# Kernel tuning notes

Measured on AMD Instinct MI355X. Metric: run time of the kernel, lower is better.

The kernel has to match this reference:

```python
import jax, jax.numpy as jnp
import numpy as np

H = 1024
W = 1024
FID = 100          # palette_fidelity
NF = 8             # number of IFS functions in the FunctionSet stub
N_POINTS = 1 << 20
K_STEPS = 20


def setup_inputs() -> dict:
    key = jax.random.key(0)
    ks = jax.random.split(key, 8)
    # xy ~ Normal(0, initial_sigma=2.0), c ~ Uniform(0,1)
    xy = 2.0 * jax.random.normal(ks[0], (N_POINTS, 2), dtype=jnp.float32)
    c = jax.random.uniform(ks[1], (N_POINTS, 1), dtype=jnp.float32)
    points = jnp.concatenate([xy, c], axis=1)                      # [N,3]
    # per-step random function selection (external FunctionSet randomness)
    choices = jax.random.randint(ks[2], (K_STEPS, N_POINTS), 0, NF, dtype=jnp.int32)
    # contractive-ish affine maps
    A = 0.5 * jax.random.normal(ks[3], (NF, 2, 2), dtype=jnp.float32)
    b = jax.random.normal(ks[4], (NF, 2), dtype=jnp.float32)
    func_colors = jax.random.uniform(ks[5], (NF,), dtype=jnp.float32)
    palette = jax.random.uniform(ks[6], (FID + 1, 4), dtype=jnp.float32)
    # view window [-3,3]x[-3,3] -> min_vec / range_vec exactly as in __init__
    x_min, x_max, y_min, y_max = -3.0, 3.0, -3.0, 3.0
    min_vec = jnp.array([x_min, y_min], dtype=jnp.float32)
    range_vec = jnp.array([W / (x_max - x_min), H / (y_max - y_min)], dtype=jnp.float32)
    raw_image0 = jnp.zeros((4, H, W), dtype=jnp.float32)
    return dict(points=points, choices=choices, A=A, b=b,
                func_colors=func_colors, palette=palette,
                min_vec=min_vec, range_vec=range_vec,
                raw_image0=raw_image0, skip_first_k=2)


def reference(points, choices, A, b, func_colors, palette,
              min_vec, range_vec, raw_image0, skip_first_k):
    def step(carry, inputs):
        pts, img = carry
        k, idx = inputs                                   # idx: [N] function ids
        xy, c = pts[:, :2], pts[:, 2]
        # FunctionSet: per-point affine map + color blend (flame IFS)
        new_xy = jnp.einsum('nij,nj->ni', A[idx], xy) + b[idx]
        new_c = 0.5 * (c + func_colors[idx])
        pts = jnp.concatenate([new_xy, new_c[:, None]], axis=1)
        # palette interpolation (matches floor/ceil lerp in the original)
        _c = new_c * FID
        cf = jnp.floor(_c)
        cc = jnp.ceil(_c)
        t = (_c - cf)[:, None]
        cfi = jnp.clip(cf, 0, FID).astype(jnp.int32)
        cci = jnp.clip(cc, 0, FID).astype(jnp.int32)
        color_vectors = t * palette[cci] + (1.0 - t) * palette[cfi]   # [N,4]
        # bin indices: ((xy - min) * range).long()  (truncation toward zero)
        bins = ((new_xy - min_vec) * range_vec).astype(jnp.int32)
        xb, yb = bins[:, 0], bins[:, 1]
        ok = (xb >= 0) & (xb < W) & (yb >= 0) & (yb < H) & (k >= skip_first_k)
        xb = jnp.where(ok, xb, 0)
        yb = jnp.where(ok, yb, 0)
        vals = jnp.where(ok[:, None], color_vectors, 0.0)             # [N,4]
        # original indexes raw_image[color][x_bins, y_bins]
        img = img.at[:, xb, yb].add(vals.T)
        return (pts, img), None

    k_steps = choices.shape[0]
    (_, img), _ = jax.lax.scan(step, (points, raw_image0),
                               (jnp.arange(k_steps), choices))
    return img
```

## Files before the change

### kernel.cpp

```cpp
#include <hip/hip_runtime.h>

constexpr int H = 1024, W = 1024, FID = 100, NF = 8;
constexpr int NPTS = 1 << 20, KSTEPS = 20;
constexpr int HW = H * W;

constexpr int NTX = 16, NTY = 32, NTILES = NTX * NTY;
constexpr int TPIX = 64 * 32;
constexpr int NBLK = 2048;
constexpr int PPB = NPTS / NBLK;
constexpr int PPT = PPB / 256;
constexpr int NBLK_C = 1024;
constexpr int SEG_N = NTILES * NBLK;
constexpr int CHUNK = 16384;
constexpr int TH    = 16384;
constexpr int MAXREC = NPTS * KSTEPS;
constexpr int K4_GRID = MAXREC / CHUNK;
constexpr int K4_BS  = 512;
constexpr int MAXVIS = K4_GRID + NTILES;
constexpr unsigned INV = 0xFFFFFFFFu;
constexpr float QSCALE = 16384.0f;
constexpr float QINV   = 1.0f / 16384.0f;
constexpr float FXS  = 131072.0f;
constexpr float FXSI = 1.0f / 131072.0f;

__device__ __forceinline__ void decode_rec(unsigned r, const float4* sPal,
                                           int& pix, float& v0, float& v1,
                                           float& v2, float& v3) {
    pix = (int)(r & 2047u);
    const float _c = (float)(r >> 11) * QINV;
    const float cf = floorf(_c);
    const float tt = _c - cf;
    const int cfi = (int)fminf(fmaxf(cf, 0.f), (float)FID);
    const int cci = (int)fminf(fmaxf(ceilf(_c), 0.f), (float)FID);
    const float4 pc = sPal[cci];
    const float4 pf = sPal[cfi];
    const float omt = 1.f - tt;
    v0 = tt * pc.x + omt * pf.x;
    v1 = tt * pc.y + omt * pf.y;
    v2 = tt * pc.z + omt * pf.z;
    v3 = tt * pc.w + omt * pf.w;
}

__device__ __forceinline__ unsigned long long pack2(float a, float b) {
    const unsigned ua = __float2uint_rn(a * FXS);
    const unsigned ub = __float2uint_rn(b * FXS);
    return (unsigned long long)ua | ((unsigned long long)ub << 32);
}

__global__ __launch_bounds__(256)
void count_kernel(const float* __restrict__ points,
                  const int* __restrict__ choices,
                  const float* __restrict__ A,
                  const float* __restrict__ b,
                  const float* __restrict__ minv,
                  const float* __restrict__ rangev,
                  const int* __restrict__ skipp,
                  unsigned* __restrict__ hist,
                  unsigned long long* __restrict__ packed)
{
    __shared__ float sA[NF * 4], sB[NF * 2];
    __shared__ unsigned shist[4][NTILES];
    const int t = threadIdx.x;
    if (t < NF * 4) sA[t] = A[t];
    if (t < NF * 2) sB[t] = b[t];
    for (int i = t; i < 4 * NTILES; i += 256) ((unsigned*)shist)[i] = 0u;
    __syncthreads();

    const int blk = blockIdx.x;
    const int base = blk * 1024;
    const int n0 = base + 4 * t;
    const float mx = minv[0], my = minv[1], rx = rangev[0], ry = rangev[1];
    const int skip = skipp[0];
    const int wv = t >> 6;

    const float4 f0 = *(const float4*)&points[3 * n0 + 0];
    const float4 f1 = *(const float4*)&points[3 * n0 + 4];
    const float4 f2 = *(const float4*)&points[3 * n0 + 8];
    float px_[4] = { f0.x, f0.w, f1.z, f2.y };
    float py_[4] = { f0.y, f1.x, f1.w, f2.z };

    unsigned long long pk_[4] = { 0ull, 0ull, 0ull, 0ull };
    unsigned ctile_[4] = { INV, INV, INV, INV };
    unsigned ccnt_[4]  = { 0u, 0u, 0u, 0u };

#pragma unroll
    for (int k = 0; k < KSTEPS; ++k) {
        const int4 cv = *(const int4*)&choices[k * NPTS + n0];
        const int idxs[4] = { cv.x & 7, cv.y & 7, cv.z & 7, cv.w & 7 };
#pragma unroll
        for (int j = 0; j < 4; ++j) {
            const int idx = idxs[j];
            pk_[j] |= (unsigned long long)idx << (3 * k);
            const float nx = sA[idx*4+0]*px_[j] + sA[idx*4+1]*py_[j] + sB[idx*2+0];
            const float ny = sA[idx*4+2]*px_[j] + sA[idx*4+3]*py_[j] + sB[idx*2+1];
            px_[j] = nx; py_[j] = ny;
            const int xb = (int)((nx - mx) * rx);
            const int yb = (int)((ny - my) * ry);
            if (k >= skip && (unsigned)xb < (unsigned)W && (unsigned)yb < (unsigned)H) {
                const unsigned tile = (unsigned)(((xb >> 6) << 5) | (yb >> 5));
                if (tile == ctile_[j]) { ++ccnt_[j]; }
                else {
                    if (ctile_[j] != INV) atomicAdd(&shist[wv][ctile_[j]], ccnt_[j]);
                    ctile_[j] = tile; ccnt_[j] = 1;
                }
            }
        }
    }
#pragma unroll
    for (int j = 0; j < 4; ++j) {
        if (ctile_[j] != INV) atomicAdd(&shist[wv][ctile_[j]], ccnt_[j]);
        packed[n0 + j] = pk_[j];
    }
    __syncthreads();
    for (int tt = t; tt < NTILES; tt += 256) {
        hist[tt * NBLK + 2 * blk]     = shist[0][tt] + shist[1][tt];
        hist[tt * NBLK + 2 * blk + 1] = shist[2][tt] + shist[3][tt];
    }
}

__global__ __launch_bounds__(1024)
void scan1_kernel(unsigned* __restrict__ hist, unsigned* __restrict__ sums)
{
    __shared__ unsigned buf[2][1024];
    const int t = threadIdx.x;
    const int base = blockIdx.x * NBLK;
    const unsigned v0 = hist[base + 2 * t];
    const unsigned v1 = hist[base + 2 * t + 1];
    int src = 0;
    buf[0][t] = v0 + v1; __syncthreads();
    for (int off = 1; off < 1024; off <<= 1) {
        unsigned val = buf[src][t];
        if (t >= off) val += buf[src][t - off];
        buf[1 - src][t] = val; src ^= 1; __syncthreads();
    }
    const unsigned incl = buf[src][t];
    const unsigned ex = incl - (v0 + v1);
    hist[base + 2 * t]     = ex;
    hist[base + 2 * t + 1] = ex + v0;
    if (t == 1023) sums[blockIdx.x] = incl;
}

__global__ __launch_bounds__(512)
void scan2v_kernel(unsigned* __restrict__ sums,
                   unsigned* __restrict__ dstart,
                   unsigned* __restrict__ vstart)
{
    __shared__ unsigned buf[2][512];
    const int t = threadIdx.x;
    const unsigned len = sums[t];

    int src = 0;
    buf[0][t] = len; __syncthreads();
    for (int off = 1; off < 512; off <<= 1) {
        unsigned val = buf[src][t];
        if (t >= off) val += buf[src][t - off];
        buf[1 - src][t] = val; src ^= 1; __syncthreads();
    }
    unsigned incl = buf[src][t];
    sums[t] = incl - len;
    if (t == 511) sums[512] = incl;

    const unsigned dlen = (len >= (unsigned)TH) ? len : 0u;
    __syncthreads();
    buf[0][t] = dlen; src = 0; __syncthreads();
    for (int off = 1; off < 512; off <<= 1) {
        unsigned val = buf[src][t];
        if (t >= off) val += buf[src][t - off];
        buf[1 - src][t] = val; src ^= 1; __syncthreads();
    }
    unsigned dincl = buf[src][t];
    const unsigned dexcl = dincl - dlen;
    dstart[t] = dexcl;
    if (t == 511) dstart[512] = dincl;

    unsigned c = 0;
    if (dlen) c = (dexcl + dlen - 1) / CHUNK - dexcl / CHUNK + 1;
    __syncthreads();
    buf[0][t] = c; src = 0; __syncthreads();
    for (int off = 1; off < 512; off <<= 1) {
        unsigned val = buf[src][t];
        if (t >= off) val += buf[src][t - off];
        buf[1 - src][t] = val; src ^= 1; __syncthreads();
    }
    unsigned vincl = buf[src][t];
    vstart[t] = vincl - c;
    if (t == 511) vstart[512] = vincl;
}

__global__ __launch_bounds__(256)
void scatter_kernel(const float* __restrict__ points,
                    const unsigned long long* __restrict__ packed,
                    const float* __restrict__ A,
                    const float* __restrict__ b,
                    const float* __restrict__ fc,
                    const float* __restrict__ minv,
                    const float* __restrict__ rangev,
                    const int* __restrict__ skipp,
                    const unsigned* __restrict__ scanb,
                    const unsigned* __restrict__ sums,
                    unsigned* __restrict__ records)
{
    __shared__ float sA[NF * 4], sB[NF * 2], sFC[NF];
    __shared__ unsigned sCur[NTILES];

    const int t = threadIdx.x;
    const int blk = blockIdx.x;
    if (t < NF * 4) sA[t] = A[t];
    if (t < NF * 2) sB[t] = b[t];
    if (t < NF)     sFC[t] = fc[t];
    for (int tt = t; tt < NTILES; tt += 256)
        sCur[tt] = scanb[tt * NBLK + blk] + sums[tt];
    __syncthreads();

    const int base = blk * PPB;
    const float mx = minv[0], my = minv[1], rx = rangev[0], ry = rangev[1];
    const int skip = skipp[0];

    for (int p = 0; p < PPT; ++p) {
        const int n = base + p * 256 + t;
        float x = points[3*n], y = points[3*n+1], c = points[3*n+2];
        const unsigned long long pk = packed[n];

#pragma unroll
        for (int k = 0; k < KSTEPS; ++k) {
            const int idx = (int)((pk >> (3 * k)) & 7ull);
            const float nx = sA[idx*4+0]*x + sA[idx*4+1]*y + sB[idx*2+0];
            const float ny = sA[idx*4+2]*x + sA[idx*4+3]*y + sB[idx*2+1];
            c = 0.5f * (c + sFC[idx]);
            x = nx; y = ny;
            const int xb = (int)((nx - mx) * rx);
            const int yb = (int)((ny - my) * ry);
            if (k >= skip && (unsigned)xb < (unsigned)W && (unsigned)yb < (unsigned)H) {
                const unsigned tile = (unsigned)(((xb >> 6) << 5) | (yb >> 5));
                const unsigned q = (unsigned)__float2int_rn(c * (100.0f * QSCALE));
                const unsigned rec = (q << 11) | (unsigned)(((xb & 63) << 5) | (yb & 31));
                const unsigned pos = atomicAdd(&sCur[tile], 1u);
                records[pos] = rec;
            }
        }
    }
}

__global__ __launch_bounds__(K4_BS)
void accum_slot_kernel(const unsigned* __restrict__ records,
                       const unsigned* __restrict__ sums,
                       const unsigned* __restrict__ dstart,
                       const unsigned* __restrict__ vstart,
                       const float* __restrict__ palette,
                       float* __restrict__ slots)
{
    __shared__ unsigned long long img01[TPIX];
    __shared__ unsigned long long img23[TPIX];
    __shared__ float4 sPal[FID + 1];
    __shared__ unsigned tstart[NTILES + 1];
    __shared__ unsigned dst[NTILES + 1];
    __shared__ unsigned vst[NTILES];
    const int t = threadIdx.x;
    for (int i = t; i < NTILES + 1; i += K4_BS) { tstart[i] = sums[i]; dst[i] = dstart[i]; }
    for (int i = t; i < NTILES; i += K4_BS) vst[i] = vstart[i];
    for (int i = t; i < (FID + 1) * 4; i += K4_BS) ((float*)sPal)[i] = palette[i];
    __syncthreads();

    const unsigned dtotal = dst[NTILES];
    const unsigned r0 = (unsigned)blockIdx.x * CHUNK;
    if (r0 >= dtotal) return;
    const unsigned r1 = min(r0 + (unsigned)CHUNK, dtotal);

    int lo = 0, hi = NTILES;
    while (lo < hi) {
        const int mid = (lo + hi + 1) >> 1;
        if (dst[mid] <= r0) lo = mid; else hi = mid - 1;
    }

    for (int tile = lo; tile < NTILES && dst[tile] < r1; ++tile) {
        const unsigned sd = max(dst[tile], r0);
        const unsigned ed = min(dst[tile + 1], r1);
        if (sd >= ed) continue;
        const unsigned gs = tstart[tile] + (sd - dst[tile]);
        const unsigned ge = gs + (ed - sd);

        for (int i = t; i < TPIX; i += K4_BS) { img01[i] = 0ull; img23[i] = 0ull; }
        __syncthreads();

        const unsigned abase = gs & ~3u;
        for (unsigned i = abase + 4u * (unsigned)t; i < ge; i += 4u * K4_BS) {
            const uint4 r4 = *(const uint4*)&records[i];
            const unsigned rr[4] = { r4.x, r4.y, r4.z, r4.w };
#pragma unroll
            for (int j = 0; j < 4; ++j) {
                const unsigned ri = i + (unsigned)j;
                if (ri >= gs && ri < ge) {
                    int pix; float v0, v1, v2, v3;
                    decode_rec(rr[j], sPal, pix, v0, v1, v2, v3);
                    atomicAdd(&img01[pix], pack2(v0, v1));
                    atomicAdd(&img23[pix], pack2(v2, v3));
                }
            }
        }
        __syncthreads();

        const unsigned slot = vst[tile] + ((unsigned)blockIdx.x - dst[tile] / CHUNK);
        float* sp = slots + (size_t)slot * (4 * TPIX);
        for (int i2 = t; i2 < TPIX; i2 += K4_BS) {
            const unsigned long long a = img01[i2];
            const unsigned long long bb = img23[i2];
            sp[0 * TPIX + i2] = (float)(unsigned)(a  & 0xFFFFFFFFu) * FXSI;
            sp[1 * TPIX + i2] = (float)(unsigned)(a  >> 32)         * FXSI;
            sp[2 * TPIX + i2] = (float)(unsigned)(bb & 0xFFFFFFFFu) * FXSI;
            sp[3 * TPIX + i2] = (float)(unsigned)(bb >> 32)         * FXSI;
        }
        __syncthreads();
    }
}

__global__ __launch_bounds__(1024)
void reduce_kernel(const float* __restrict__ slots,
                   const unsigned* __restrict__ vstart,
                   const unsigned* __restrict__ sums,
                   const unsigned* __restrict__ records,
                   const float* __restrict__ palette,
                   const float* __restrict__ raw0,
                   float* __restrict__ out)
{
    __shared__ unsigned long long l01[TPIX];
    __shared__ unsigned long long l23[TPIX];
    __shared__ float4 sPal[FID + 1];
    const int T = blockIdx.x;
    const int t = threadIdx.x;
    for (int i = t; i < (FID + 1) * 4; i += 1024) ((float*)sPal)[i] = palette[i];

    const unsigned v0 = vstart[T], v1 = vstart[T + 1];
    const unsigned s = sums[T], e = sums[T + 1];
    const bool sparse = (v0 == v1) && (e > s);
    if (sparse) for (int i = t; i < TPIX; i += 1024) { l01[i] = 0ull; l23[i] = 0ull; }
    __syncthreads();

    float4 acc0 = {0.f,0.f,0.f,0.f}, acc1 = {0.f,0.f,0.f,0.f};
    for (unsigned v = v0; v < v1; ++v) {
        const float4* sp = (const float4*)(slots + (size_t)v * (4 * TPIX));
        const float4 a = sp[t];
        const float4 bq = sp[t + 1024];
        acc0.x += a.x;  acc0.y += a.y;  acc0.z += a.z;  acc0.w += a.w;
        acc1.x += bq.x; acc1.y += bq.y; acc1.z += bq.z; acc1.w += bq.w;
    }

    if (sparse) {
        for (unsigned i = s + t; i < e; i += 1024) {
            int pix; float w0, w1, w2, w3;
            decode_rec(records[i], sPal, pix, w0, w1, w2, w3);
            atomicAdd(&l01[pix], pack2(w0, w1));
            atomicAdd(&l23[pix], pack2(w2, w3));
        }
    }
    __syncthreads();

    const int tx = T >> 5, ty = T & 31;
#pragma unroll
    for (int half = 0; half < 2; ++half) {
        const int f  = t + half * 1024;
        const int ch = f >> 9;
        const int q  = f & 511;
        const int p0 = q * 4;
        float4 acc = half ? acc1 : acc0;
        if (sparse) {
#pragma unroll
            for (int j = 0; j < 4; ++j) {
                const int p = p0 + j;
                float vadd;
                if (ch == 0)      vadd = (float)(unsigned)(l01[p] & 0xFFFFFFFFu) * FXSI;
                else if (ch == 1) vadd = (float)(unsigned)(l01[p] >> 32) * FXSI;
                else if (ch == 2) vadd = (float)(unsigned)(l23[p] & 0xFFFFFFFFu) * FXSI;
                else              vadd = (float)(unsigned)(l23[p] >> 32) * FXSI;
                if (j == 0) acc.x += vadd;
                else if (j == 1) acc.y += vadd;
                else if (j == 2) acc.z += vadd;
                else acc.w += vadd;
            }
        }
        const int px = p0 >> 5, py = p0 & 31;
        const size_t o = (size_t)ch * HW + (size_t)(tx * 64 + px) * W + (ty * 32 + py);
        const float4 r = *(const float4*)(raw0 + o);
        acc.x += r.x; acc.y += r.y; acc.z += r.z; acc.w += r.w;
        *(float4*)(out + o) = acc;
    }
}

__global__ __launch_bounds__(256)
void flame_kernel_planar(const float* __restrict__ points,
                         const int* __restrict__ choices,
                         const float* __restrict__ A,
                         const float* __restrict__ b,
                         const float* __restrict__ fc,
                         const float* __restrict__ palette,
                         const float* __restrict__ min_vec,
                         const float* __restrict__ range_vec,
                         const int* __restrict__ skipp,
                         float* __restrict__ out)
{
    __shared__ float sA[NF * 4];
    __shared__ float sB[NF * 2];
    __shared__ float sFC[NF];
    __shared__ float4 sPal[FID + 1];
    const int t = threadIdx.x;
    if (t < NF * 4) sA[t] = A[t];
    if (t < NF * 2) sB[t] = b[t];
    if (t < NF)     sFC[t] = fc[t];
    for (int i = t; i < (FID + 1) * 4; i += 256) ((float*)sPal)[i] = palette[i];
    __syncthreads();

    const int n = blockIdx.x * 256 + t;
    float x = points[3 * n], y = points[3 * n + 1], c = points[3 * n + 2];
    const float mx = min_vec[0], my = min_vec[1];
    const float rx = range_vec[0], ry = range_vec[1];
    const int skip = skipp[0];

    for (int k = 0; k < KSTEPS; ++k) {
        const int idx = choices[k * NPTS + n];
        const float nx = sA[idx*4+0]*x + sA[idx*4+1]*y + sB[idx*2+0];
        const float ny = sA[idx*4+2]*x + sA[idx*4+3]*y + sB[idx*2+1];
        c = 0.5f * (c + sFC[idx]);
        x = nx; y = ny;
        const float _c = c * (float)FID;
        const float cf = floorf(_c);
        const float tt = _c - cf;
        const int cfi = (int)fminf(fmaxf(cf, 0.f), (float)FID);
        const int cci = (int)fminf(fmaxf(ceilf(_c), 0.f), (float)FID);
        const float4 pc = sPal[cci];
        const float4 pf = sPal[cfi];
        const int xb = (int)((nx - mx) * rx);
        const int yb = (int)((ny - my) * ry);
        if (k >= skip && (unsigned)xb < (unsigned)W && (unsigned)yb < (unsigned)H) {
            const int p = xb * W + yb;
            const float omt = 1.f - tt;
            atomicAdd(out + p + 0 * HW, tt * pc.x + omt * pf.x);
            atomicAdd(out + p + 1 * HW, tt * pc.y + omt * pf.y);
            atomicAdd(out + p + 2 * HW, tt * pc.z + omt * pf.z);
            atomicAdd(out + p + 3 * HW, tt * pc.w + omt * pf.w);
        }
    }
}

extern "C" void kernel_launch(void* const* d_in, const int* in_sizes, int n_in,
                              void* d_out, int out_size, void* d_ws, size_t ws_size,
                              hipStream_t stream) {
    const float* points    = (const float*)d_in[0];
    const int*   choices   = (const int*)d_in[1];
    const float* A         = (const float*)d_in[2];
    const float* b         = (const float*)d_in[3];
    const float* fc        = (const float*)d_in[4];
    const float* palette   = (const float*)d_in[5];
    const float* min_vec   = (const float*)d_in[6];
    const float* range_vec = (const float*)d_in[7];
    const float* raw0      = (const float*)d_in[8];
    const int*   skipp     = (const int*)d_in[9];
    float* out = (float*)d_out;
    const size_t img_bytes = (size_t)4 * HW * sizeof(float);

    const size_t rec_off  = 0;
    const size_t rec_cap  = (size_t)MAXREC * 4;
    const size_t sums_off = rec_off + rec_cap;
    const size_t dst_off  = sums_off + 4096;
    const size_t vst_off  = dst_off + 4096;
    const size_t slot_off = vst_off + 4096;
    const size_t slot_cap = (size_t)MAXVIS * (4 * TPIX) * sizeof(float);
    const size_t pk_off   = slot_off;
    const size_t hist_off = slot_off + (size_t)NPTS * 8;
    const size_t need1    = slot_off + slot_cap;

    unsigned* sums = (unsigned*)((char*)d_ws + sums_off);
    unsigned* recs = (unsigned*)((char*)d_ws + rec_off);

    if (ws_size >= need1) {
        unsigned* hist   = (unsigned*)((char*)d_ws + hist_off);
        unsigned* dstart = (unsigned*)((char*)d_ws + dst_off);
        unsigned* vstart = (unsigned*)((char*)d_ws + vst_off);
        float*    slots  = (float*)((char*)d_ws + slot_off);
        unsigned long long* packed = (unsigned long long*)((char*)d_ws + pk_off);

        count_kernel<<<NBLK_C, 256, 0, stream>>>(
            points, choices, A, b, min_vec, range_vec, skipp, hist, packed);
        scan1_kernel<<<NTILES, 1024, 0, stream>>>(hist, sums);
        scan2v_kernel<<<1, 512, 0, stream>>>(sums, dstart, vstart);
        scatter_kernel<<<NBLK, 256, 0, stream>>>(
            points, packed, A, b, fc, min_vec, range_vec, skipp, hist, sums, recs);
        accum_slot_kernel<<<K4_GRID, K4_BS, 0, stream>>>(
            recs, sums, dstart, vstart, palette, slots);
        reduce_kernel<<<NTILES, 1024, 0, stream>>>(
            slots, vstart, sums, recs, palette, raw0, out);
    } else {
        hipMemcpyAsync(out, raw0, img_bytes, hipMemcpyDeviceToDevice, stream);
        flame_kernel_planar<<<NPTS / 256, 256, 0, stream>>>(
            points, choices, A, b, fc, palette, min_vec, range_vec, skipp, out);
    }
}
```

Baseline: 307.5 us.

## Replicate per-block tile cursors four ways to reduce LDS atomic contention

Splits each block's per-tile histogram and scatter cursor into four copies, with threads assigned to copies by a lane-based hash. The counting histogram, the scan layout and the scatter cursor initialisation all change so each copy gets its own contiguous segment in the record array. The aim is to cut same-address shared-memory atomic conflicts during scatter, where many points land in the same tile. In exchange the histogram becomes four times larger and the first scan pass reads eight values per thread.

```diff
diff --git a/kernel.cpp b/kernel.cpp
--- a/kernel.cpp
+++ b/kernel.cpp
@@ -10,7 +10,8 @@
 constexpr int PPB = NPTS / NBLK;
 constexpr int PPT = PPB / 256;
 constexpr int NBLK_C = 1024;
-constexpr int SEG_N = NTILES * NBLK;
+constexpr int NCPY = 4;
+constexpr int HSTR = NBLK * NCPY;
 constexpr int CHUNK = 16384;
 constexpr int TH    = 16384;
 constexpr int MAXREC = NPTS * KSTEPS;
@@ -59,11 +60,11 @@
                   unsigned long long* __restrict__ packed)
 {
     __shared__ float sA[NF * 4], sB[NF * 2];
-    __shared__ unsigned shist[4][NTILES];
+    __shared__ unsigned shist[4][NCPY][NTILES];
     const int t = threadIdx.x;
     if (t < NF * 4) sA[t] = A[t];
     if (t < NF * 2) sB[t] = b[t];
-    for (int i = t; i < 4 * NTILES; i += 256) ((unsigned*)shist)[i] = 0u;
+    for (int i = t; i < 4 * NCPY * NTILES; i += 256) ((unsigned*)shist)[i] = 0u;
     __syncthreads();
 
     const int blk = blockIdx.x;
@@ -100,7 +101,8 @@
                 const unsigned tile = (unsigned)(((xb >> 6) << 5) | (yb >> 5));
                 if (tile == ctile_[j]) { ++ccnt_[j]; }
                 else {
-                    if (ctile_[j] != INV) atomicAdd(&shist[wv][ctile_[j]], ccnt_[j]);
+                    if (ctile_[j] != INV)
+                        atomicAdd(&shist[wv][(t + j) & 3][ctile_[j]], ccnt_[j]);
                     ctile_[j] = tile; ccnt_[j] = 1;
                 }
             }
@@ -108,13 +110,16 @@
     }
 #pragma unroll
     for (int j = 0; j < 4; ++j) {
-        if (ctile_[j] != INV) atomicAdd(&shist[wv][ctile_[j]], ccnt_[j]);
+        if (ctile_[j] != INV) atomicAdd(&shist[wv][(t + j) & 3][ctile_[j]], ccnt_[j]);
         packed[n0 + j] = pk_[j];
     }
     __syncthreads();
     for (int tt = t; tt < NTILES; tt += 256) {
-        hist[tt * NBLK + 2 * blk]     = shist[0][tt] + shist[1][tt];
-        hist[tt * NBLK + 2 * blk + 1] = shist[2][tt] + shist[3][tt];
+#pragma unroll
+        for (int c = 0; c < NCPY; ++c) {
+            hist[(size_t)tt * HSTR + (2 * blk)     * NCPY + c] = shist[0][c][tt] + shist[1][c][tt];
+            hist[(size_t)tt * HSTR + (2 * blk + 1) * NCPY + c] = shist[2][c][tt] + shist[3][c][tt];
+        }
     }
 }
 
@@ -123,20 +128,22 @@
 {
     __shared__ unsigned buf[2][1024];
     const int t = threadIdx.x;
-    const int base = blockIdx.x * NBLK;
-    const unsigned v0 = hist[base + 2 * t];
-    const unsigned v1 = hist[base + 2 * t + 1];
+    const size_t base = (size_t)blockIdx.x * HSTR;
+    unsigned v[8];
+    unsigned s = 0;
+#pragma unroll
+    for (int j = 0; j < 8; ++j) { v[j] = hist[base + 8 * t + j]; s += v[j]; }
     int src = 0;
-    buf[0][t] = v0 + v1; __syncthreads();
+    buf[0][t] = s; __syncthreads();
     for (int off = 1; off < 1024; off <<= 1) {
         unsigned val = buf[src][t];
         if (t >= off) val += buf[src][t - off];
         buf[1 - src][t] = val; src ^= 1; __syncthreads();
     }
     const unsigned incl = buf[src][t];
-    const unsigned ex = incl - (v0 + v1);
-    hist[base + 2 * t]     = ex;
-    hist[base + 2 * t + 1] = ex + v0;
+    unsigned ex = incl - s;
+#pragma unroll
+    for (int j = 0; j < 8; ++j) { hist[base + 8 * t + j] = ex; ex += v[j]; }
     if (t == 1023) sums[blockIdx.x] = incl;
 }
 
@@ -201,20 +208,26 @@
                     unsigned* __restrict__ records)
 {
     __shared__ float sA[NF * 4], sB[NF * 2], sFC[NF];
-    __shared__ unsigned sCur[NTILES];
+    __shared__ unsigned sCur[NCPY * NTILES];
 
     const int t = threadIdx.x;
     const int blk = blockIdx.x;
     if (t < NF * 4) sA[t] = A[t];
     if (t < NF * 2) sB[t] = b[t];
     if (t < NF)     sFC[t] = fc[t];
-    for (int tt = t; tt < NTILES; tt += 256)
-        sCur[tt] = scanb[tt * NBLK + blk] + sums[tt];
+    for (int i = t; i < NCPY * NTILES; i += 256) {
+        const int tile = i & (NTILES - 1);
+        const int c = i >> 9;
+        sCur[c * NTILES + tile] =
+            scanb[(size_t)tile * HSTR + blk * NCPY + c] + sums[tile];
+    }
     __syncthreads();
 
     const int base = blk * PPB;
     const float mx = minv[0], my = minv[1], rx = rangev[0], ry = rangev[1];
     const int skip = skipp[0];
+    const int cpy = ((t >> 2) + (t & 3)) & 3;
+    unsigned* const myCur = &sCur[cpy * NTILES];
 
     for (int p = 0; p < PPT; ++p) {
         const int n = base + p * 256 + t;
@@ -234,7 +247,7 @@
                 const unsigned tile = (unsigned)(((xb >> 6) << 5) | (yb >> 5));
                 const unsigned q = (unsigned)__float2int_rn(c * (100.0f * QSCALE));
                 const unsigned rec = (q << 11) | (unsigned)(((xb & 63) << 5) | (yb & 31));
-                const unsigned pos = atomicAdd(&sCur[tile], 1u);
+                const unsigned pos = atomicAdd(&myCur[tile], 1u);
                 records[pos] = rec;
             }
         }
```

Result: slower. 367.7 us (+19.6%).
